# Optimization experiments

Hardware: AMD Instinct MI355X
Metric: run time of the kernel (lower is better)

Reference implementation:

```python
import jax, jax.numpy as jnp
import numpy as np

# Routing structure from the torch module
GT0 = [[0,1,0,0,1,0],[0,1,0,0,0,1],[0,0,1,0,1,0],[0,0,1,0,0,1],[0,0,0,1,1,0],[0,0,0,1,0,1]]
NCLS = 6
K = 1  # top-k

def _expert_pairs():
    # For class i, expert index m = 1+(j-1)*5+(k-1) maps to atom1[j-1] -> atom2[k-1].
    pairs = []
    for i in range(NCLS):
        p = [(j - 1, k - 1) for j in range(1, 6) for k in range(1, 6)
             if j != k and GT0[i][j] == 1 and GT0[i][k] == 1]
        pairs.append(p)
    return pairs

PAIRS = _expert_pairs()  # each class has exactly 2 (atom1, atom2) pairs

B, P, D, H = 64, 256, 768, 3072

def setup_inputs() -> dict:
    key = jax.random.key(0)
    ks = jax.random.split(key, 8)
    s = 0.02
    x = jax.random.normal(ks[0], (B, NCLS + P, D), dtype=jnp.float32)
    mids = jax.random.randint(ks[1], (B,), 0, 6)
    moe0_W1 = jax.random.normal(ks[2], (D, H), dtype=jnp.float32) * s
    moe0_b1 = jnp.zeros((H,), jnp.float32)
    moe0_W2 = jax.random.normal(ks[3], (H, D), dtype=jnp.float32) * s
    moe0_b2 = jnp.zeros((D,), jnp.float32)
    A1_W = jax.random.normal(ks[4], (5, D, H), dtype=jnp.float32) * s  # atom1 linears
    A1_b = jnp.zeros((5, H), jnp.float32)
    A2_W = jax.random.normal(ks[5], (5, H, D), dtype=jnp.float32) * s  # atom2 linears
    A2_b = jnp.zeros((5, D), jnp.float32)
    G_W = jax.random.normal(ks[6], (NCLS, D, 2), dtype=jnp.float32) * s  # per-class gates (2 experts each, no bias)
    return {"x": x, "moe0_W1": moe0_W1, "moe0_b1": moe0_b1, "moe0_W2": moe0_W2,
            "moe0_b2": moe0_b2, "A1_W": A1_W, "A1_b": A1_b, "A2_W": A2_W,
            "A2_b": A2_b, "G_W": G_W, "mids": mids}

def _gelu(t):
    return jax.nn.gelu(t, approximate=False)  # torch nn.GELU default = erf

def reference(x, moe0_W1, moe0_b1, moe0_W2, moe0_b2, A1_W, A1_b, A2_W, A2_b, G_W, mids):
    cls_tokens = x[:, :NCLS]          # [B, 6, D]
    patch_tokens = x[:, NCLS:]        # [B, P, D]
    patch_out = _gelu(patch_tokens @ moe0_W1 + moe0_b1) @ moe0_W2 + moe0_b2  # [B, P, D]
    cls_outs = []
    for i in range(NCLS):
        tok = cls_tokens[:, i]        # [B, D]
        eouts = [ _gelu(tok @ A1_W[a] + A1_b[a]) @ A2_W[c] + A2_b[c] for (a, c) in PAIRS[i] ]
        out = jnp.stack(eouts, axis=-1)                 # [B, D, E=2]
        gate = jax.nn.softmax(tok @ G_W[i], axis=-1)    # [B, E]
        # top-k masking (k=1 < E=2): keep gates strictly above the (k+1)-th largest
        thr = jnp.sort(gate, axis=-1)[..., -(K + 1)]    # [B]
        mask = (gate > thr[..., None]).astype(gate.dtype)
        g = gate * mask
        g = g / jnp.clip(jnp.sum(g, axis=-1, keepdims=True), 1e-6)
        cls_outs.append(jnp.sum(out * g[:, None, :], axis=-1))  # [B, D]
    cls_out = jnp.stack(cls_outs, axis=1)               # [B, 6, D]
    return jnp.concatenate([cls_out, patch_out], axis=1)  # [B, 6+P, D]
```

## Files before the change

### kernel.cpp

```cpp
#include <hip/hip_runtime.h>
#include <hip/hip_bf16.h>

#define DD 768
#define HH 3072
#define BB 64
#define TT 262
#define NCLS6 6

typedef __bf16 bf16x8 __attribute__((ext_vector_type(8)));
typedef float f32x4 __attribute__((ext_vector_type(4)));

__device__ __constant__ int A_FIRST[12]  = {0,3, 0,4, 1,3, 1,4, 2,3, 2,4};
__device__ __constant__ int A_SECOND[12] = {3,0, 4,0, 3,1, 4,1, 3,2, 4,2};

__device__ __forceinline__ float gelu_f(float x) {
  return 0.5f * x * (1.0f + erff(x * 0.70710678118654752f));
}

__device__ __forceinline__ void load_lds16(const void* g, void* l) {
  __builtin_amdgcn_global_load_lds(
      (const __attribute__((address_space(1))) void*)g,
      (__attribute__((address_space(3))) void*)l,
      16, 0, 0);
}

__global__ void cast_x_kernel(const float* __restrict__ in, __hip_bfloat16* __restrict__ out, int n4) {
  int i = blockIdx.x * blockDim.x + threadIdx.x;
  if (i < n4) {
    float4 v = ((const float4*)in)[i];
    __hip_bfloat16* o = out + (size_t)i * 4;
    o[0] = __float2bfloat16(v.x);
    o[1] = __float2bfloat16(v.y);
    o[2] = __float2bfloat16(v.z);
    o[3] = __float2bfloat16(v.w);
  }
}

__global__ void transpose_cast(const float* __restrict__ in, __hip_bfloat16* __restrict__ out, int R, int C) {
  __shared__ __hip_bfloat16 tile[32][33];
  size_t boff = (size_t)blockIdx.z * R * C;
  const float* ip = in + boff;
  __hip_bfloat16* op = out + boff;
  int c0 = blockIdx.x * 32, r0 = blockIdx.y * 32;
  int tx = threadIdx.x & 31;
  int ty = threadIdx.x >> 5;
#pragma unroll
  for (int s = 0; s < 4; ++s) {
    int rr = ty * 4 + s;
    tile[rr][tx] = __float2bfloat16(ip[(size_t)(r0 + rr) * C + c0 + tx]);
  }
  __syncthreads();
#pragma unroll
  for (int s = 0; s < 4; ++s) {
    int cc = ty * 4 + s;
    op[(size_t)(c0 + cc) * R + r0 + tx] = tile[tx][cc];
  }
}

__global__ void gate_kernel(const float* __restrict__ x, const float* __restrict__ GW, int* __restrict__ sel) {
  int b = blockIdx.x, i = blockIdx.y;
  int lane = threadIdx.x;
  const float* tok = x + (size_t)(b * TT + i) * DD;
  const float* g = GW + (size_t)i * DD * 2;
  float p0 = 0.f, p1 = 0.f;
  for (int k = lane; k < DD; k += 64) {
    float t = tok[k];
    p0 += t * g[k * 2 + 0];
    p1 += t * g[k * 2 + 1];
  }
#pragma unroll
  for (int o = 32; o; o >>= 1) { p0 += __shfl_xor(p0, o); p1 += __shfl_xor(p1, o); }
  if (lane == 0) sel[i * 64 + b] = (p0 > p1) ? 0 : ((p1 > p0) ? 1 : 2);
}

__global__ void finalize_cls(const float* __restrict__ part, const float* __restrict__ A2b,
                             const int* __restrict__ sel, float* __restrict__ out) {
  int t = blockIdx.x * blockDim.x + threadIdx.x;
  int d4 = t % 192;
  int b = (t / 192) & 63;
  int cls = t / (192 * 64);
  int s = sel[cls * 64 + b];
  float4 res = make_float4(0.f, 0.f, 0.f, 0.f);
  if (s != 2) {
    int combo = cls * 2 + s;
    const float4* bb = (const float4*)(A2b + (size_t)A_SECOND[combo] * DD);
    res = bb[d4];
#pragma unroll
    for (int z = 0; z < 4; ++z) {
      const float4* p = (const float4*)(part + (((size_t)z * 12 + combo) * 64 + b) * DD);
      float4 v = p[d4];
      res.x += v.x; res.y += v.y; res.z += v.z; res.w += v.w;
    }
  }
  ((float4*)out)[(size_t)(b * TT + cls) * 192 + d4] = res;
}

template <int BM, int MODE>
__global__ __launch_bounds__(256, 2)
void gemm_k(const __hip_bfloat16* __restrict__ A,
            const __hip_bfloat16* __restrict__ Bw,
            const float* __restrict__ bias,
            void* __restrict__ Out,
            const int* __restrict__ sel) {
  constexpr int BN = 128;
  constexpr int KDIM = (MODE == 0 || MODE == 2) ? DD : HH;
  constexpr int KITERS = (MODE == 3) ? 12 : KDIM / 64;
  constexpr int WAVES_M = (BM == 128) ? 2 : 1;
  constexpr int WAVES_N = 4 / WAVES_M;
  constexpr int MT = BM / (16 * WAVES_M);
  constexpr int NT = BN / (16 * WAVES_N);
  constexpr int CHA = BM / 32;
  constexpr int CHB = BN / 32;

  __shared__ __align__(16) char smem[(BM + BN) * 128];
  char* As = smem;
  char* Bs = smem + BM * 128;

  const int tid = threadIdx.x;
  const int lane = tid & 63;
  const int wave = tid >> 6;
  const int q = lane >> 4;
  const int r = lane & 15;
  const int wave_m = wave / WAVES_N;
  const int wave_n = wave % WAVES_N;

  int m0 = 0, n0, combo = 0, cls_i = 0, zsp = 0;
  size_t k0b = 0;
  const __hip_bfloat16* Bp = Bw;
  const float* biasp = bias;
  if constexpr (MODE == 0) {
    int l = blockIdx.x;
    int xcd = l & 7;
    int i = l >> 3;
    int mb = i / 3;
    int nloc = i - mb * 3;
    m0 = mb * BM;
    n0 = (xcd * 3 + nloc) * BN;
  } else if constexpr (MODE == 1) {
    m0 = blockIdx.x * BM;
    n0 = blockIdx.y * BN;
  } else {
    n0 = blockIdx.x * BN;
    combo = blockIdx.y;
    cls_i = combo >> 1;
    int e = (MODE == 2) ? A_FIRST[combo] : A_SECOND[combo];
    Bp = Bw + (size_t)e * DD * HH;
    if constexpr (MODE == 2) biasp = bias + e * HH;
    if constexpr (MODE == 3) { zsp = blockIdx.z; k0b = (size_t)zsp * 768 * 2; }
  }

  const char* gA[CHA];
  const char* gB[CHB];
#pragma unroll
  for (int u = 0; u < CHA; ++u) {
    int c = u * 256 + tid;
    int row = c >> 3;
    int within = ((c & 7) ^ (row & 7)) * 16;
    size_t rowoff;
    if constexpr (MODE == 0) {
      int m = m0 + row;
      int b = m >> 8, p = m & 255;
      rowoff = (size_t)(b * TT + 6 + p) * DD * 2;
    } else if constexpr (MODE == 1) {
      rowoff = (size_t)(m0 + row) * HH * 2;
    } else if constexpr (MODE == 2) {
      rowoff = (size_t)(row * TT + cls_i) * DD * 2;
    } else {
      rowoff = (size_t)(combo * 64 + row) * HH * 2 + k0b;
    }
    gA[u] = (const char*)A + rowoff + within;
  }
#pragma unroll
  for (int u = 0; u < CHB; ++u) {
    int c = u * 256 + tid;
    int row = c >> 3;
    int within = ((c & 7) ^ (row & 7)) * 16;
    gB[u] = (const char*)Bp + (size_t)(n0 + row) * KDIM * 2 + k0b + within;
  }
  const int wave_base = (tid & ~63) * 16;

  f32x4 acc[MT][NT];
#pragma unroll
  for (int i_ = 0; i_ < MT; ++i_)
#pragma unroll
    for (int j_ = 0; j_ < NT; ++j_) acc[i_][j_] = (f32x4){0.f, 0.f, 0.f, 0.f};

  const int rx = r & 7;
  const int sa = (q ^ rx) * 16;
  const char* a_rd0 = As + (wave_m * MT * 16 + r) * 128 + sa;
  const char* a_rd1 = As + (wave_m * MT * 16 + r) * 128 + (sa ^ 64);
  const char* b_rd0 = Bs + (wave_n * NT * 16 + r) * 128 + sa;
  const char* b_rd1 = Bs + (wave_n * NT * 16 + r) * 128 + (sa ^ 64);

  for (int kt = 0; kt < KITERS; ++kt) {
#pragma unroll
    for (int u = 0; u < CHA; ++u) {
      load_lds16(gA[u], As + u * 4096 + wave_base);
      gA[u] += 128;
    }
#pragma unroll
    for (int u = 0; u < CHB; ++u) {
      load_lds16(gB[u], Bs + u * 4096 + wave_base);
      gB[u] += 128;
    }
    __syncthreads();
    bf16x8 af0[MT], af1[MT], bf0[NT], bf1[NT];
#pragma unroll
    for (int i_ = 0; i_ < MT; ++i_) {
      af0[i_] = *(const bf16x8*)(a_rd0 + i_ * 2048);
      af1[i_] = *(const bf16x8*)(a_rd1 + i_ * 2048);
    }
#pragma unroll
    for (int j_ = 0; j_ < NT; ++j_) {
      bf0[j_] = *(const bf16x8*)(b_rd0 + j_ * 2048);
      bf1[j_] = *(const bf16x8*)(b_rd1 + j_ * 2048);
    }
#pragma unroll
    for (int i_ = 0; i_ < MT; ++i_)
#pragma unroll
      for (int j_ = 0; j_ < NT; ++j_)
        acc[i_][j_] = __builtin_amdgcn_mfma_f32_16x16x32_bf16(af0[i_], bf0[j_], acc[i_][j_], 0, 0, 0);
#pragma unroll
    for (int i_ = 0; i_ < MT; ++i_)
#pragma unroll
      for (int j_ = 0; j_ < NT; ++j_)
        acc[i_][j_] = __builtin_amdgcn_mfma_f32_16x16x32_bf16(af1[i_], bf1[j_], acc[i_][j_], 0, 0, 0);
    __syncthreads();
  }

#pragma unroll
  for (int i_ = 0; i_ < MT; ++i_) {
#pragma unroll
    for (int j_ = 0; j_ < NT; ++j_) {
      int n_g = n0 + (wave_n * NT + j_) * 16 + r;
      float bb = 0.f;
      if constexpr (MODE != 3) bb = biasp[n_g];
      f32x4 v = acc[i_][j_];
#pragma unroll
      for (int rg = 0; rg < 4; ++rg) {
        int m_g = m0 + (wave_m * MT + i_) * 16 + q * 4 + rg;
        float val = v[rg] + bb;
        if constexpr (MODE == 0) {
          ((__hip_bfloat16*)Out)[(size_t)m_g * HH + n_g] = __float2bfloat16(gelu_f(val));
        } else if constexpr (MODE == 1) {
          int b = m_g >> 8, p = m_g & 255;
          ((float*)Out)[(size_t)(b * TT + 6 + p) * DD + n_g] = val;
        } else if constexpr (MODE == 2) {
          ((__hip_bfloat16*)Out)[(size_t)(combo * 64 + m_g) * HH + n_g] = __float2bfloat16(gelu_f(val));
        } else {
          ((float*)Out)[(((size_t)zsp * 12 + combo) * 64 + m_g) * DD + n_g] = val;
        }
      }
    }
  }
}

extern "C" void kernel_launch(void* const* d_in, const int* in_sizes, int n_in,
                              void* d_out, int out_size, void* d_ws, size_t ws_size,
                              hipStream_t stream) {
  const float* x   = (const float*)d_in[0];
  const float* W1  = (const float*)d_in[1];
  const float* b1  = (const float*)d_in[2];
  const float* W2  = (const float*)d_in[3];
  const float* b2  = (const float*)d_in[4];
  const float* A1W = (const float*)d_in[5];
  const float* A1b = (const float*)d_in[6];
  const float* A2W = (const float*)d_in[7];
  const float* A2b = (const float*)d_in[8];
  const float* GW  = (const float*)d_in[9];
  float* out = (float*)d_out;

  char* ws = (char*)d_ws;
  __hip_bfloat16* xb   = (__hip_bfloat16*)(ws + 0);
  __hip_bfloat16* W1t  = (__hip_bfloat16*)(ws + 25755648);
  __hip_bfloat16* W2t  = (__hip_bfloat16*)(ws + 30474240);
  __hip_bfloat16* A1t  = (__hip_bfloat16*)(ws + 35192832);
  __hip_bfloat16* A2t  = (__hip_bfloat16*)(ws + 58785792);
  __hip_bfloat16* hcls = (__hip_bfloat16*)(ws + 82378752);
  int* sel             = (int*)(ws + 87097344);
  __hip_bfloat16* hid  = (__hip_bfloat16*)(ws + 87099136);
  float* part          = (float*)(ws + 35192832);

  cast_x_kernel<<<12576, 256, 0, stream>>>(x, xb, 3219456);
  transpose_cast<<<dim3(96, 24, 1), 256, 0, stream>>>(W1, W1t, DD, HH);
  transpose_cast<<<dim3(24, 96, 1), 256, 0, stream>>>(W2, W2t, HH, DD);
  transpose_cast<<<dim3(96, 24, 5), 256, 0, stream>>>(A1W, A1t, DD, HH);
  transpose_cast<<<dim3(24, 96, 5), 256, 0, stream>>>(A2W, A2t, HH, DD);
  gate_kernel<<<dim3(64, 6), 64, 0, stream>>>(x, GW, sel);

  gemm_k<64, 2><<<dim3(24, 12), 256, 0, stream>>>(xb, A1t, A1b, hcls, nullptr);
  gemm_k<64, 3><<<dim3(6, 12, 4), 256, 0, stream>>>(hcls, A2t, nullptr, part, nullptr);
  finalize_cls<<<288, 256, 0, stream>>>(part, A2b, sel, out);

  gemm_k<128, 0><<<3072, 256, 0, stream>>>(xb, W1t, b1, hid, nullptr);
  gemm_k<128, 1><<<dim3(128, 6), 256, 0, stream>>>(hid, W2t, b2, out, nullptr);
}
```

Baseline: 439.1 us.

## Widen GEMM tiles, swap MFMA operands for vector epilogue, fast GELU, merge transposes

Several changes land together. The patch GEMM1 now uses 128x256 tiles with a simple row-major block order in place of the XCD-aware swizzle. MFMA operands are swapped so each lane holds four consecutive columns, which lets the epilogue write vectorized bf16x4 and float4 stores with vector bias loads. The erf GELU is replaced by a tanh-style exp approximation with a manual bf16 round, and the four weight transpose launches are merged into two. The approximate GELU changes numerics, and the larger tile raises register and LDS pressure, which may lower occupancy.

```diff
diff --git a/kernel.cpp b/kernel.cpp
--- a/kernel.cpp
+++ b/kernel.cpp
@@ -5,16 +5,23 @@
 #define HH 3072
 #define BB 64
 #define TT 262
-#define NCLS6 6
 
 typedef __bf16 bf16x8 __attribute__((ext_vector_type(8)));
 typedef float f32x4 __attribute__((ext_vector_type(4)));
+typedef unsigned short u16;
+typedef unsigned int u32;
 
 __device__ __constant__ int A_FIRST[12]  = {0,3, 0,4, 1,3, 1,4, 2,3, 2,4};
 __device__ __constant__ int A_SECOND[12] = {3,0, 4,0, 3,1, 4,1, 3,2, 4,2};
 
 __device__ __forceinline__ float gelu_f(float x) {
-  return 0.5f * x * (1.0f + erff(x * 0.70710678118654752f));
+  float n2t = x * fmaf(x * x, -0.0713548163f, -1.5957691216f);
+  return x * __builtin_amdgcn_rcpf(1.0f + __expf(n2t));
+}
+
+__device__ __forceinline__ u16 f2bf(float x) {
+  u32 u = __builtin_bit_cast(u32, x);
+  return (u16)((u + 0x7fffu + ((u >> 16) & 1u)) >> 16);
 }
 
 __device__ __forceinline__ void load_lds16(const void* g, void* l) {
@@ -28,19 +35,20 @@
   int i = blockIdx.x * blockDim.x + threadIdx.x;
   if (i < n4) {
     float4 v = ((const float4*)in)[i];
-    __hip_bfloat16* o = out + (size_t)i * 4;
-    o[0] = __float2bfloat16(v.x);
-    o[1] = __float2bfloat16(v.y);
-    o[2] = __float2bfloat16(v.z);
-    o[3] = __float2bfloat16(v.w);
-  }
-}
-
-__global__ void transpose_cast(const float* __restrict__ in, __hip_bfloat16* __restrict__ out, int R, int C) {
+    u16* o = (u16*)out + (size_t)i * 4;
+    union { u16 s[4]; uint2 d; } pk;
+    pk.s[0] = f2bf(v.x); pk.s[1] = f2bf(v.y); pk.s[2] = f2bf(v.z); pk.s[3] = f2bf(v.w);
+    *(uint2*)o = pk.d;
+  }
+}
+
+__global__ void transpose_cast6(const float* __restrict__ w, const float* __restrict__ a,
+                                __hip_bfloat16* __restrict__ wt, __hip_bfloat16* __restrict__ at,
+                                int R, int C) {
   __shared__ __hip_bfloat16 tile[32][33];
-  size_t boff = (size_t)blockIdx.z * R * C;
-  const float* ip = in + boff;
-  __hip_bfloat16* op = out + boff;
+  int z = blockIdx.z;
+  const float* ip = z ? (a + (size_t)(z - 1) * R * C) : w;
+  __hip_bfloat16* op = z ? (at + (size_t)(z - 1) * R * C) : wt;
   int c0 = blockIdx.x * 32, r0 = blockIdx.y * 32;
   int tx = threadIdx.x & 31;
   int ty = threadIdx.x >> 5;
@@ -95,14 +103,13 @@
   ((float4*)out)[(size_t)(b * TT + cls) * 192 + d4] = res;
 }
 
-template <int BM, int MODE>
+template <int BM, int BN, int MODE>
 __global__ __launch_bounds__(256, 2)
 void gemm_k(const __hip_bfloat16* __restrict__ A,
             const __hip_bfloat16* __restrict__ Bw,
             const float* __restrict__ bias,
             void* __restrict__ Out,
             const int* __restrict__ sel) {
-  constexpr int BN = 128;
   constexpr int KDIM = (MODE == 0 || MODE == 2) ? DD : HH;
   constexpr int KITERS = (MODE == 3) ? 12 : KDIM / 64;
   constexpr int WAVES_M = (BM == 128) ? 2 : 1;
@@ -129,16 +136,13 @@
   const __hip_bfloat16* Bp = Bw;
   const float* biasp = bias;
   if constexpr (MODE == 0) {
-    int l = blockIdx.x;
-    int xcd = l & 7;
-    int i = l >> 3;
-    int mb = i / 3;
-    int nloc = i - mb * 3;
-    m0 = mb * BM;
-    n0 = (xcd * 3 + nloc) * BN;
+    int bx = blockIdx.x;
+    m0 = (bx / 12) * BM;
+    n0 = (bx % 12) * BN;
   } else if constexpr (MODE == 1) {
-    m0 = blockIdx.x * BM;
-    n0 = blockIdx.y * BN;
+    int bx = blockIdx.x;
+    m0 = (bx / 6) * BM;
+    n0 = (bx % 6) * BN;
   } else {
     n0 = blockIdx.x * BN;
     combo = blockIdx.y;
@@ -149,34 +153,23 @@
     if constexpr (MODE == 3) { zsp = blockIdx.z; k0b = (size_t)zsp * 768 * 2; }
   }
 
-  const char* gA[CHA];
-  const char* gB[CHB];
-#pragma unroll
-  for (int u = 0; u < CHA; ++u) {
-    int c = u * 256 + tid;
-    int row = c >> 3;
-    int within = ((c & 7) ^ (row & 7)) * 16;
-    size_t rowoff;
-    if constexpr (MODE == 0) {
-      int m = m0 + row;
-      int b = m >> 8, p = m & 255;
-      rowoff = (size_t)(b * TT + 6 + p) * DD * 2;
-    } else if constexpr (MODE == 1) {
-      rowoff = (size_t)(m0 + row) * HH * 2;
-    } else if constexpr (MODE == 2) {
-      rowoff = (size_t)(row * TT + cls_i) * DD * 2;
-    } else {
-      rowoff = (size_t)(combo * 64 + row) * HH * 2 + k0b;
-    }
-    gA[u] = (const char*)A + rowoff + within;
-  }
-#pragma unroll
-  for (int u = 0; u < CHB; ++u) {
-    int c = u * 256 + tid;
-    int row = c >> 3;
-    int within = ((c & 7) ^ (row & 7)) * 16;
-    gB[u] = (const char*)Bp + (size_t)(n0 + row) * KDIM * 2 + k0b + within;
-  }
+  const int trow = tid >> 3;
+  const int sw = ((tid & 7) ^ (trow & 7)) << 4;
+  size_t a_row_off;
+  if constexpr (MODE == 0) {
+    int m = m0 + trow;
+    a_row_off = (size_t)((m >> 8) * TT + 6 + (m & 255)) * DD * 2;
+  } else if constexpr (MODE == 1) {
+    a_row_off = (size_t)(m0 + trow) * HH * 2;
+  } else if constexpr (MODE == 2) {
+    a_row_off = (size_t)(trow * TT + cls_i) * DD * 2;
+  } else {
+    a_row_off = (size_t)(combo * 64 + trow) * HH * 2 + k0b;
+  }
+  const char* gA0 = (const char*)A + a_row_off + sw;
+  const char* gB0 = (const char*)Bp + (size_t)(n0 + trow) * KDIM * 2 + k0b + sw;
+  constexpr size_t ASTR = (size_t)32 * ((MODE == 0) ? DD : (MODE == 2) ? TT * DD : HH) * 2;
+  constexpr size_t BSTR = (size_t)32 * KDIM * 2;
   const int wave_base = (tid & ~63) * 16;
 
   f32x4 acc[MT][NT];
@@ -185,71 +178,61 @@
 #pragma unroll
     for (int j_ = 0; j_ < NT; ++j_) acc[i_][j_] = (f32x4){0.f, 0.f, 0.f, 0.f};
 
-  const int rx = r & 7;
-  const int sa = (q ^ rx) * 16;
-  const char* a_rd0 = As + (wave_m * MT * 16 + r) * 128 + sa;
-  const char* a_rd1 = As + (wave_m * MT * 16 + r) * 128 + (sa ^ 64);
-  const char* b_rd0 = Bs + (wave_n * NT * 16 + r) * 128 + sa;
-  const char* b_rd1 = Bs + (wave_n * NT * 16 + r) * 128 + (sa ^ 64);
+  const char* a_rd = As + (wave_m * (MT * 16) + r) * 128;
+  const char* b_rd = Bs + (wave_n * (NT * 16) + r) * 128;
+  const int sa = ((q ^ (r & 7)) << 4);
 
   for (int kt = 0; kt < KITERS; ++kt) {
 #pragma unroll
-    for (int u = 0; u < CHA; ++u) {
-      load_lds16(gA[u], As + u * 4096 + wave_base);
-      gA[u] += 128;
-    }
-#pragma unroll
-    for (int u = 0; u < CHB; ++u) {
-      load_lds16(gB[u], Bs + u * 4096 + wave_base);
-      gB[u] += 128;
+    for (int u = 0; u < CHA; ++u) load_lds16(gA0 + u * ASTR, As + u * 4096 + wave_base);
+#pragma unroll
+    for (int u = 0; u < CHB; ++u) load_lds16(gB0 + u * BSTR, Bs + u * 4096 + wave_base);
+    gA0 += 128;
+    gB0 += 128;
+    __syncthreads();
+#pragma unroll
+    for (int t = 0; t < 2; ++t) {
+      const int so = sa ^ (t << 6);
+      bf16x8 af[MT], bf[NT];
+#pragma unroll
+      for (int i_ = 0; i_ < MT; ++i_) af[i_] = *(const bf16x8*)(a_rd + i_ * 2048 + so);
+#pragma unroll
+      for (int j_ = 0; j_ < NT; ++j_) bf[j_] = *(const bf16x8*)(b_rd + j_ * 2048 + so);
+#pragma unroll
+      for (int i_ = 0; i_ < MT; ++i_)
+#pragma unroll
+        for (int j_ = 0; j_ < NT; ++j_)
+          acc[i_][j_] = __builtin_amdgcn_mfma_f32_16x16x32_bf16(bf[j_], af[i_], acc[i_][j_], 0, 0, 0);
     }
     __syncthreads();
-    bf16x8 af0[MT], af1[MT], bf0[NT], bf1[NT];
-#pragma unroll
-    for (int i_ = 0; i_ < MT; ++i_) {
-      af0[i_] = *(const bf16x8*)(a_rd0 + i_ * 2048);
-      af1[i_] = *(const bf16x8*)(a_rd1 + i_ * 2048);
-    }
+  }
+
+#pragma unroll
+  for (int i_ = 0; i_ < MT; ++i_) {
+    int m_g = m0 + wave_m * (MT * 16) + i_ * 16 + r;
 #pragma unroll
     for (int j_ = 0; j_ < NT; ++j_) {
-      bf0[j_] = *(const bf16x8*)(b_rd0 + j_ * 2048);
-      bf1[j_] = *(const bf16x8*)(b_rd1 + j_ * 2048);
-    }
-#pragma unroll
-    for (int i_ = 0; i_ < MT; ++i_)
-#pragma unroll
-      for (int j_ = 0; j_ < NT; ++j_)
-        acc[i_][j_] = __builtin_amdgcn_mfma_f32_16x16x32_bf16(af0[i_], bf0[j_], acc[i_][j_], 0, 0, 0);
-#pragma unroll
-    for (int i_ = 0; i_ < MT; ++i_)
-#pragma unroll
-      for (int j_ = 0; j_ < NT; ++j_)
-        acc[i_][j_] = __builtin_amdgcn_mfma_f32_16x16x32_bf16(af1[i_], bf1[j_], acc[i_][j_], 0, 0, 0);
-    __syncthreads();
-  }
-
-#pragma unroll
-  for (int i_ = 0; i_ < MT; ++i_) {
-#pragma unroll
-    for (int j_ = 0; j_ < NT; ++j_) {
-      int n_g = n0 + (wave_n * NT + j_) * 16 + r;
-      float bb = 0.f;
-      if constexpr (MODE != 3) bb = biasp[n_g];
+      int nb = n0 + wave_n * (NT * 16) + j_ * 16 + q * 4;
       f32x4 v = acc[i_][j_];
-#pragma unroll
-      for (int rg = 0; rg < 4; ++rg) {
-        int m_g = m0 + (wave_m * MT + i_) * 16 + q * 4 + rg;
-        float val = v[rg] + bb;
-        if constexpr (MODE == 0) {
-          ((__hip_bfloat16*)Out)[(size_t)m_g * HH + n_g] = __float2bfloat16(gelu_f(val));
-        } else if constexpr (MODE == 1) {
-          int b = m_g >> 8, p = m_g & 255;
-          ((float*)Out)[(size_t)(b * TT + 6 + p) * DD + n_g] = val;
-        } else if constexpr (MODE == 2) {
-          ((__hip_bfloat16*)Out)[(size_t)(combo * 64 + m_g) * HH + n_g] = __float2bfloat16(gelu_f(val));
-        } else {
-          ((float*)Out)[(((size_t)zsp * 12 + combo) * 64 + m_g) * DD + n_g] = val;
-        }
+      if constexpr (MODE != 3) {
+        f32x4 bb = *(const f32x4*)(biasp + nb);
+        v += bb;
+      }
+      if constexpr (MODE == 0) {
+        union { u16 s[4]; uint2 d; } pk;
+#pragma unroll
+        for (int rg = 0; rg < 4; ++rg) pk.s[rg] = f2bf(gelu_f(v[rg]));
+        *(uint2*)((u16*)Out + (size_t)m_g * HH + nb) = pk.d;
+      } else if constexpr (MODE == 1) {
+        int b = m_g >> 8, p = m_g & 255;
+        *(f32x4*)((float*)Out + (size_t)(b * TT + 6 + p) * DD + nb) = v;
+      } else if constexpr (MODE == 2) {
+        union { u16 s[4]; uint2 d; } pk;
+#pragma unroll
+        for (int rg = 0; rg < 4; ++rg) pk.s[rg] = f2bf(gelu_f(v[rg]));
+        *(uint2*)((u16*)Out + (size_t)(combo * 64 + m_g) * HH + nb) = pk.d;
+      } else {
+        *(f32x4*)((float*)Out + (((size_t)zsp * 12 + combo) * 64 + m_g) * DD + nb) = v;
       }
     }
   }
@@ -282,16 +265,14 @@
   float* part          = (float*)(ws + 35192832);
 
   cast_x_kernel<<<12576, 256, 0, stream>>>(x, xb, 3219456);
-  transpose_cast<<<dim3(96, 24, 1), 256, 0, stream>>>(W1, W1t, DD, HH);
-  transpose_cast<<<dim3(24, 96, 1), 256, 0, stream>>>(W2, W2t, HH, DD);
-  transpose_cast<<<dim3(96, 24, 5), 256, 0, stream>>>(A1W, A1t, DD, HH);
-  transpose_cast<<<dim3(24, 96, 5), 256, 0, stream>>>(A2W, A2t, HH, DD);
+  transpose_cast6<<<dim3(96, 24, 6), 256, 0, stream>>>(W1, A1W, W1t, A1t, DD, HH);
+  transpose_cast6<<<dim3(24, 96, 6), 256, 0, stream>>>(W2, A2W, W2t, A2t, HH, DD);
   gate_kernel<<<dim3(64, 6), 64, 0, stream>>>(x, GW, sel);
 
-  gemm_k<64, 2><<<dim3(24, 12), 256, 0, stream>>>(xb, A1t, A1b, hcls, nullptr);
-  gemm_k<64, 3><<<dim3(6, 12, 4), 256, 0, stream>>>(hcls, A2t, nullptr, part, nullptr);
+  gemm_k<64, 128, 2><<<dim3(24, 12), 256, 0, stream>>>(xb, A1t, A1b, hcls, nullptr);
+  gemm_k<64, 128, 3><<<dim3(6, 12, 4), 256, 0, stream>>>(hcls, A2t, nullptr, part, nullptr);
   finalize_cls<<<288, 256, 0, stream>>>(part, A2b, sel, out);
 
-  gemm_k<128, 0><<<3072, 256, 0, stream>>>(xb, W1t, b1, hid, nullptr);
-  gemm_k<128, 1><<<dim3(128, 6), 256, 0, stream>>>(hid, W2t, b2, out, nullptr);
-}
+  gemm_k<128, 256, 0><<<1536, 256, 0, stream>>>(xb, W1t, b1, hid, nullptr);
+  gemm_k<128, 128, 1><<<768, 256, 0, stream>>>(hid, W2t, b2, out, nullptr);
+}
```

Result: slower. 448.5 us (+2.1%).
